# Performance work log

Hardware: AMD Instinct MI355X
Metric: run time of the kernel (lower is better)

## Reference

```python
import jax, jax.numpy as jnp
import numpy as np

B, T, E, D = 64, 512, 1024, 1024  # batch, enc timesteps, enc hidden, dec hidden


def setup_inputs() -> dict:
    key = jax.random.key(0)
    ks = jax.random.split(key, 9)
    s = lambda fan_in: 1.0 / np.sqrt(fan_in)
    return {
        "hidden": jax.random.normal(ks[0], (B, D), jnp.float32),
        "decoder_out": jax.random.normal(ks[1], (B, D), jnp.float32),
        "encoder_states": jax.random.normal(ks[2], (T, B, E), jnp.float32),
        # attn: Linear(D+E -> 2E)
        "Wa": jax.random.uniform(ks[3], (2 * E, D + E), jnp.float32, -s(D + E), s(D + E)),
        "ba": jax.random.uniform(ks[4], (2 * E,), jnp.float32, -s(D + E), s(D + E)),
        # attn2: Linear(2E -> 1)
        "w2": jax.random.uniform(ks[5], (1, 2 * E), jnp.float32, -s(2 * E), s(2 * E)),
        "b2": jax.random.uniform(ks[6], (1,), jnp.float32, -s(2 * E), s(2 * E)),
        # attn_combine: Linear(D+E -> D)
        "Wc": jax.random.uniform(ks[7], (D, D + E), jnp.float32, -s(D + E), s(D + E)),
        "bc": jax.random.uniform(ks[8], (D,), jnp.float32, -s(D + E), s(D + E)),
    }


def reference(hidden, decoder_out, encoder_states, Wa, ba, w2, b2, Wc, bc):
    d = hidden.shape[1]
    # attn(cat(hidden, enc_t)) = hidden @ Wa[:, :D].T + enc_t @ Wa[:, D:].T + ba
    h_proj = hidden @ Wa[:, :d].T + ba                      # [B, 2E]
    e_proj = jnp.einsum('tbe,fe->tbf', encoder_states, Wa[:, d:])  # [T, B, 2E]
    act = jnp.tanh(h_proj[None, :, :] + e_proj)             # [T, B, 2E]
    scores = jnp.einsum('tbf,f->bt', act, w2[0]) + b2[0]    # [B, T]
    weights = jax.nn.softmax(scores, axis=-1)               # softmax over timesteps
    # weighted sum of encoder states: [B, E]
    applied = jnp.einsum('bt,tbe->be', weights, encoder_states)
    combined = jnp.concatenate([decoder_out, applied], axis=1)  # [B, D+E]
    out = jnp.tanh(combined @ Wc.T + bc)                    # [B, D]
    return out, applied
```

## Files before the change

### kernel.cpp

```cpp
#include <hip/hip_runtime.h>
#include <hip/hip_bf16.h>

#define BB 64
#define TT 512
#define EE 1024
#define DD 1024

typedef __attribute__((ext_vector_type(8))) short s16x8;
typedef __attribute__((ext_vector_type(4))) float f32x4;

#define AS1 __attribute__((address_space(1)))
#define AS3 __attribute__((address_space(3)))

__device__ __forceinline__ unsigned short f2bf(float f) {
    unsigned int u = __builtin_bit_cast(unsigned int, f);
    u += 0x7FFF + ((u >> 16) & 1);
    return (unsigned short)(u >> 16);
}
__device__ __forceinline__ float tanh_fast(float x) {
    x = fminf(fmaxf(x, -15.f), 15.f);
    float e = __expf(2.f * x);
    return (e - 1.f) / (e + 1.f);
}

__device__ __forceinline__ int tile_slot(int row, int g) {
    return (row >> 4) * 128 + (g >> 2) * 64 + (g & 3) * 16 + (row & 15);
}

__global__ __launch_bounds__(256) void conv_encS_kernel(
    const float* __restrict__ enc, unsigned short* __restrict__ encS)
{
    __shared__ short tileL[1024 * 8];
    const int tm  = blockIdx.x;
    const int tk  = blockIdx.y;
    const int tid = threadIdx.x;

#pragma unroll
    for (int it = 0; it < 4; ++it) {
        int cidx = it * 256 + tid;
        int row  = cidx >> 3;
        int g    = cidx & 7;
        const float* src = enc + (size_t)(tm * 128 + row) * 1024 + tk * 64 + g * 8;
        float4 v0 = ((const float4*)src)[0];
        float4 v1 = ((const float4*)src)[1];
        short c[8];
        c[0] = (short)f2bf(v0.x); c[1] = (short)f2bf(v0.y);
        c[2] = (short)f2bf(v0.z); c[3] = (short)f2bf(v0.w);
        c[4] = (short)f2bf(v1.x); c[5] = (short)f2bf(v1.y);
        c[6] = (short)f2bf(v1.z); c[7] = (short)f2bf(v1.w);
        *(s16x8*)&tileL[tile_slot(row, g) * 8] = *(s16x8*)c;
    }
    __syncthreads();
    unsigned short* dst = encS + ((size_t)tm * 16 + tk) * 8192;
#pragma unroll
    for (int it = 0; it < 4; ++it) {
        int s = it * 256 + tid;
        *(s16x8*)&dst[s * 8] = *(const s16x8*)&tileL[s * 8];
    }
}

__global__ __launch_bounds__(256) void prep_kernel(
    const float* __restrict__ Wa,
    const float* __restrict__ hidden,
    const float* __restrict__ ba,
    unsigned short* __restrict__ WaS,
    float* __restrict__ hp)
{
    __shared__ float smem[8 * 1024];
    const int bid = blockIdx.x;
    const int tid = threadIdx.x;

    if (bid < 256) {
        short* tileL = (short*)smem;
        const int tn = bid & 15;
        const int tk = bid >> 4;
#pragma unroll
        for (int it = 0; it < 4; ++it) {
            int cidx = it * 256 + tid;
            int row  = cidx >> 3;
            int g    = cidx & 7;
            const float* src = Wa + (size_t)(tn * 128 + row) * 2048 + 1024 + tk * 64 + g * 8;
            float4 v0 = ((const float4*)src)[0];
            float4 v1 = ((const float4*)src)[1];
            short c[8];
            c[0] = (short)f2bf(v0.x); c[1] = (short)f2bf(v0.y);
            c[2] = (short)f2bf(v0.z); c[3] = (short)f2bf(v0.w);
            c[4] = (short)f2bf(v1.x); c[5] = (short)f2bf(v1.y);
            c[6] = (short)f2bf(v1.z); c[7] = (short)f2bf(v1.w);
            *(s16x8*)&tileL[tile_slot(row, g) * 8] = *(s16x8*)c;
        }
        __syncthreads();
        unsigned short* dst = WaS + ((size_t)tn * 16 + tk) * 8192;
#pragma unroll
        for (int it = 0; it < 4; ++it) {
            int s = it * 256 + tid;
            *(s16x8*)&dst[s * 8] = *(const s16x8*)&tileL[s * 8];
        }
    } else {
        const int lane = tid & 63;
        const int wave = tid >> 6;
        const int f0   = (bid - 256) * 8;
#pragma unroll
        for (int i = 0; i < 8; ++i) {
            int idx = i * 256 + tid;
            int fi  = idx >> 8;
            int c4  = idx & 255;
            ((float4*)smem)[idx] = *(const float4*)(Wa + (size_t)(f0 + fi) * 2048 + c4 * 4);
        }
        __syncthreads();
        for (int bi = 0; bi < 16; ++bi) {
            int b = wave * 16 + bi;
            float h[16];
#pragma unroll
            for (int j = 0; j < 16; ++j) h[j] = hidden[b * 1024 + lane + 64 * j];
#pragma unroll
            for (int fi = 0; fi < 8; ++fi) {
                float s = 0.f;
#pragma unroll
                for (int j = 0; j < 16; ++j) s += h[j] * smem[fi * 1024 + lane + 64 * j];
#pragma unroll
                for (int m = 32; m; m >>= 1) s += __shfl_xor(s, m);
                if (lane == 0) hp[(f0 + fi) * 64 + b] = s + ba[f0 + fi];
            }
        }
    }
}

__global__ __launch_bounds__(1024) void gemm_scores(
    const unsigned short* __restrict__ encS,
    const unsigned short* __restrict__ WaS,
    const float* __restrict__ hp,
    const float* __restrict__ w2,
    float* __restrict__ scoresP)
{
    __shared__ short sA[2][2][8192];
    __shared__ short sB[2][2][8192];
    __shared__ float rowAcc[256];

    const int tid  = threadIdx.x;
    const int bid  = blockIdx.x;
    const int w    = (bid & 7) * 128 + (bid >> 3);
    const int bm   = w >> 3;
    const int bn   = w & 7;
    const int lane = tid & 63;
    const int wave = tid >> 6;
    const int wm   = wave >> 2;
    const int wn   = wave & 3;
    const int c    = lane & 15;
    const int quad = lane >> 4;
    const int mt   = wm >> 1;
    const int mrow0 = (wm & 1) * 4;
    const int nt   = wn >> 1;
    const int nrow0 = (wn & 1) * 4;

    f32x4 acc[4][4];
#pragma unroll
    for (int m = 0; m < 4; ++m)
#pragma unroll
        for (int n = 0; n < 4; ++n)
#pragma unroll
            for (int r = 0; r < 4; ++r) acc[m][n][r] = 0.f;

    const unsigned short* aT = encS + ((size_t)(bm * 2) * 16) * 8192;
    const unsigned short* bT = WaS  + ((size_t)(bn * 2) * 16) * 8192;

    auto STAGE_ALL = [&](int kt, int nb) {
#pragma unroll
        for (int t = 0; t < 2; ++t) {
            const unsigned short* sa = aT + ((size_t)(t * 16 + kt)) * 8192;
            __builtin_amdgcn_global_load_lds(
                (const AS1 void*)(sa + tid * 8),
                (AS3 void*)&sA[nb][t][tid * 8], 16, 0, 0);
            const unsigned short* sb = bT + ((size_t)(t * 16 + kt)) * 8192;
            __builtin_amdgcn_global_load_lds(
                (const AS1 void*)(sb + tid * 8),
                (AS3 void*)&sB[nb][t][tid * 8], 16, 0, 0);
        }
    };

    STAGE_ALL(0, 0);

    for (int kt = 0; kt < 16; ++kt) {
        const int cur = kt & 1;
        asm volatile("s_waitcnt vmcnt(0)" ::: "memory");
        __builtin_amdgcn_s_barrier();
        __builtin_amdgcn_sched_barrier(0);
        if (kt < 15) STAGE_ALL(kt + 1, cur ^ 1);

#pragma unroll
        for (int kk = 0; kk < 2; ++kk) {
            s16x8 aF[4], bF[4];
#pragma unroll
            for (int m = 0; m < 4; ++m)
                aF[m] = *(const s16x8*)
                    &sA[cur][mt][((mrow0 + m) * 128 + kk * 64 + lane) * 8];
#pragma unroll
            for (int n = 0; n < 4; ++n)
                bF[n] = *(const s16x8*)
                    &sB[cur][nt][((nrow0 + n) * 128 + kk * 64 + lane) * 8];

            __builtin_amdgcn_s_setprio(1);
#pragma unroll
            for (int m = 0; m < 4; ++m)
#pragma unroll
                for (int n = 0; n < 4; ++n)
                    acc[m][n] = __builtin_amdgcn_mfma_f32_16x16x32_bf16(
                        aF[m], bF[n], acc[m][n], 0, 0, 0);
            __builtin_amdgcn_s_setprio(0);
        }
        __builtin_amdgcn_sched_barrier(0);
        __builtin_amdgcn_s_barrier();
    }

    if (tid < 256) rowAcc[tid] = 0.f;
    __syncthreads();

    float w2v[4];
#pragma unroll
    for (int n = 0; n < 4; ++n) w2v[n] = w2[bn * 256 + wn * 64 + n * 16 + c];

#pragma unroll
    for (int m = 0; m < 4; ++m) {
        int lrow0 = wm * 64 + m * 16 + quad * 4;
        int b0    = lrow0 & 63;
        f32x4 hp4[4];
#pragma unroll
        for (int n = 0; n < 4; ++n)
            hp4[n] = *(const f32x4*)&hp[(bn * 256 + wn * 64 + n * 16 + c) * 64 + b0];
#pragma unroll
        for (int r = 0; r < 4; ++r) {
            float s = 0.f;
#pragma unroll
            for (int n = 0; n < 4; ++n)
                s += tanh_fast(acc[m][n][r] + hp4[n][r]) * w2v[n];
            s += __shfl_xor(s, 1);
            s += __shfl_xor(s, 2);
            s += __shfl_xor(s, 4);
            s += __shfl_xor(s, 8);
            if (c == 0) atomicAdd(&rowAcc[lrow0 + r], s);
        }
    }
    __syncthreads();
    if (tid < 256) {
        int b = tid & 63;
        int t = bm * 4 + (tid >> 6);
        scoresP[((size_t)bn * 64 + b) * 512 + t] = rowAcc[tid];
    }
}

__global__ __launch_bounds__(256) void applied_part_kernel(
    const float* __restrict__ enc,
    const float* __restrict__ scoresP,
    float* __restrict__ part)
{
    __shared__ float red[128 * 8];
    __shared__ float sw[512];
    __shared__ float red4[4];
    const int tc  = blockIdx.x;
    const int b   = blockIdx.y;
    const int tid = threadIdx.x;
    const int eo  = tid & 127;
    const int th  = tid >> 7;
    const int e0  = eo * 8;

    {
        const int t0 = tid * 2;
        float s0 = 0.f, s1 = 0.f;
#pragma unroll
        for (int bn = 0; bn < 8; ++bn) {
            const float* sp = scoresP + ((size_t)bn * 64 + b) * 512;
            s0 += sp[t0]; s1 += sp[t0 + 1];
        }
        float m = fmaxf(s0, s1);
#pragma unroll
        for (int o = 32; o; o >>= 1) m = fmaxf(m, __shfl_xor(m, o));
        if ((tid & 63) == 0) red4[tid >> 6] = m;
        __syncthreads();
        m = fmaxf(fmaxf(red4[0], red4[1]), fmaxf(red4[2], red4[3]));
        __syncthreads();
        float e0v = __expf(s0 - m), e1v = __expf(s1 - m);
        float ss = e0v + e1v;
#pragma unroll
        for (int o = 32; o; o >>= 1) ss += __shfl_xor(ss, o);
        if ((tid & 63) == 0) red4[tid >> 6] = ss;
        __syncthreads();
        float inv = 1.f / (red4[0] + red4[1] + red4[2] + red4[3]);
        sw[t0]     = e0v * inv;
        sw[t0 + 1] = e1v * inv;
        __syncthreads();
    }

    float a[8];
#pragma unroll
    for (int j = 0; j < 8; ++j) a[j] = 0.f;

    for (int it = 0; it < 16; ++it) {
        int t = tc * 32 + th * 16 + it;
        float wt = sw[t];
        const float* src = enc + ((size_t)(t * BB + b)) * EE + e0;
        float4 v0 = ((const float4*)src)[0];
        float4 v1 = ((const float4*)src)[1];
        a[0] += wt * v0.x; a[1] += wt * v0.y; a[2] += wt * v0.z; a[3] += wt * v0.w;
        a[4] += wt * v1.x; a[5] += wt * v1.y; a[6] += wt * v1.z; a[7] += wt * v1.w;
    }
    if (th == 1) {
#pragma unroll
        for (int j = 0; j < 8; ++j) red[eo * 8 + j] = a[j];
    }
    __syncthreads();
    if (th == 0) {
        float* dst = part + ((size_t)tc * 64 + b) * 1024 + e0;
#pragma unroll
        for (int j = 0; j < 8; ++j) dst[j] = a[j] + red[eo * 8 + j];
    }
}

__global__ __launch_bounds__(256) void applied_reduce_kernel(
    const float* __restrict__ part, float* __restrict__ out_applied)
{
    int idx = blockIdx.x * 256 + threadIdx.x;
    float s = 0.f;
#pragma unroll
    for (int tc = 0; tc < 16; ++tc) s += part[tc * 65536 + idx];
    out_applied[idx] = s;
}

__global__ __launch_bounds__(256) void combine_kernel(
    const float* __restrict__ dec,
    const float* applied,
    const float* __restrict__ Wc,
    const float* __restrict__ bc,
    float* out0)
{
    const int gw   = blockIdx.x * 4 + (threadIdx.x >> 6);
    const int lane = threadIdx.x & 63;
    const int d0   = (gw >> 3) * 8;
    const int b0   = (gw & 7) * 8;

    float acc[8][8];
#pragma unroll
    for (int dd = 0; dd < 8; ++dd)
#pragma unroll
        for (int bb = 0; bb < 8; ++bb) acc[dd][bb] = 0.f;

#pragma unroll
    for (int j = 0; j < 8; ++j) {
        float4 wv[8];
#pragma unroll
        for (int dd = 0; dd < 8; ++dd)
            wv[dd] = ((const float4*)(Wc + (size_t)(d0 + dd) * 2048))[j * 64 + lane];
        float4 cv[8];
        if (j < 4) {
#pragma unroll
            for (int bb = 0; bb < 8; ++bb)
                cv[bb] = ((const float4*)(dec + (size_t)(b0 + bb) * 1024))[j * 64 + lane];
        } else {
#pragma unroll
            for (int bb = 0; bb < 8; ++bb)
                cv[bb] = ((const float4*)(applied + (size_t)(b0 + bb) * 1024))[(j - 4) * 64 + lane];
        }
#pragma unroll
        for (int dd = 0; dd < 8; ++dd)
#pragma unroll
            for (int bb = 0; bb < 8; ++bb)
                acc[dd][bb] += wv[dd].x * cv[bb].x + wv[dd].y * cv[bb].y
                             + wv[dd].z * cv[bb].z + wv[dd].w * cv[bb].w;
    }

#pragma unroll
    for (int dd = 0; dd < 8; ++dd) {
#pragma unroll
        for (int bb = 0; bb < 8; ++bb) {
            float s = acc[dd][bb];
#pragma unroll
            for (int m = 32; m; m >>= 1) s += __shfl_xor(s, m);
            if (lane == 0)
                out0[(size_t)(b0 + bb) * DD + d0 + dd] = tanh_fast(s + bc[d0 + dd]);
        }
    }
}

extern "C" void kernel_launch(void* const* d_in, const int* in_sizes, int n_in,
                              void* d_out, int out_size, void* d_ws, size_t ws_size,
                              hipStream_t stream) {
    const float* hidden = (const float*)d_in[0];
    const float* dec    = (const float*)d_in[1];
    const float* enc    = (const float*)d_in[2];
    const float* Wa     = (const float*)d_in[3];
    const float* ba     = (const float*)d_in[4];
    const float* w2     = (const float*)d_in[5];
    const float* Wc     = (const float*)d_in[7];
    const float* bc     = (const float*)d_in[8];
    float* out = (float*)d_out;

    unsigned short* encS = (unsigned short*)d_ws;
    unsigned short* WaS  = encS + (size_t)33554432;
    float* hp      = (float*)(WaS + (size_t)2097152);
    float* scoresP = hp + 131072;
    float* part    = scoresP + 262144;

    dim3 gc(256, 16);
    conv_encS_kernel<<<gc, 256, 0, stream>>>(enc, encS);
    prep_kernel<<<512, 256, 0, stream>>>(Wa, hidden, ba, WaS, hp);
    gemm_scores<<<1024, 1024, 0, stream>>>(encS, WaS, hp, w2, scoresP);
    dim3 g3(16, 64);
    applied_part_kernel<<<g3, 256, 0, stream>>>(enc, scoresP, part);
    applied_reduce_kernel<<<256, 256, 0, stream>>>(part, out + BB * DD);
    combine_kernel<<<256, 256, 0, stream>>>(dec, out + BB * DD, Wc, bc, out);
}
```

Before: 515.2 us.

## Fuse encoder fp32-to-bf16 conversion into GEMM A-tile staging

Removes the separate conversion kernel that wrote a bf16 swizzled copy of encoder_states to workspace. The GEMM now loads fp32 encoder rows into registers, converts them to bf16 and writes them into LDS in the swizzled tile layout, pipelined one k-step ahead. B tiles still use direct global-to-LDS loads. This avoids a full extra write and read pass over the 128 MB encoder tensor, in exchange for doubled A global traffic per GEMM block (fp32, and each A tile is reread by the 8 N-blocks), extra register pressure and conversion ALU work inside the main loop.

```diff
diff --git a/kernel.cpp b/kernel.cpp
--- a/kernel.cpp
+++ b/kernel.cpp
@@ -25,38 +25,6 @@
 
 __device__ __forceinline__ int tile_slot(int row, int g) {
     return (row >> 4) * 128 + (g >> 2) * 64 + (g & 3) * 16 + (row & 15);
-}
-
-__global__ __launch_bounds__(256) void conv_encS_kernel(
-    const float* __restrict__ enc, unsigned short* __restrict__ encS)
-{
-    __shared__ short tileL[1024 * 8];
-    const int tm  = blockIdx.x;
-    const int tk  = blockIdx.y;
-    const int tid = threadIdx.x;
-
-#pragma unroll
-    for (int it = 0; it < 4; ++it) {
-        int cidx = it * 256 + tid;
-        int row  = cidx >> 3;
-        int g    = cidx & 7;
-        const float* src = enc + (size_t)(tm * 128 + row) * 1024 + tk * 64 + g * 8;
-        float4 v0 = ((const float4*)src)[0];
-        float4 v1 = ((const float4*)src)[1];
-        short c[8];
-        c[0] = (short)f2bf(v0.x); c[1] = (short)f2bf(v0.y);
-        c[2] = (short)f2bf(v0.z); c[3] = (short)f2bf(v0.w);
-        c[4] = (short)f2bf(v1.x); c[5] = (short)f2bf(v1.y);
-        c[6] = (short)f2bf(v1.z); c[7] = (short)f2bf(v1.w);
-        *(s16x8*)&tileL[tile_slot(row, g) * 8] = *(s16x8*)c;
-    }
-    __syncthreads();
-    unsigned short* dst = encS + ((size_t)tm * 16 + tk) * 8192;
-#pragma unroll
-    for (int it = 0; it < 4; ++it) {
-        int s = it * 256 + tid;
-        *(s16x8*)&dst[s * 8] = *(const s16x8*)&tileL[s * 8];
-    }
 }
 
 __global__ __launch_bounds__(256) void prep_kernel(
@@ -127,7 +95,7 @@
 }
 
 __global__ __launch_bounds__(1024) void gemm_scores(
-    const unsigned short* __restrict__ encS,
+    const float* __restrict__ enc,
     const unsigned short* __restrict__ WaS,
     const float* __restrict__ hp,
     const float* __restrict__ w2,
@@ -153,6 +121,11 @@
     const int nt   = wn >> 1;
     const int nrow0 = (wn & 1) * 4;
 
+    const int arow  = tid >> 3;
+    const int ag    = tid & 7;
+    const int aslot = tile_slot(arow, ag) * 8;
+    const float* aBase = enc + ((size_t)(bm * 256) + arow) * 1024 + ag * 8;
+
     f32x4 acc[4][4];
 #pragma unroll
     for (int m = 0; m < 4; ++m)
@@ -161,16 +134,32 @@
 #pragma unroll
             for (int r = 0; r < 4; ++r) acc[m][n][r] = 0.f;
 
-    const unsigned short* aT = encS + ((size_t)(bm * 2) * 16) * 8192;
-    const unsigned short* bT = WaS  + ((size_t)(bn * 2) * 16) * 8192;
-
-    auto STAGE_ALL = [&](int kt, int nb) {
+    const unsigned short* bT = WaS + ((size_t)(bn * 2) * 16) * 8192;
+
+    float4 pa[2][2];
+
+    auto A_LOAD = [&](int kt) {
 #pragma unroll
         for (int t = 0; t < 2; ++t) {
-            const unsigned short* sa = aT + ((size_t)(t * 16 + kt)) * 8192;
-            __builtin_amdgcn_global_load_lds(
-                (const AS1 void*)(sa + tid * 8),
-                (AS3 void*)&sA[nb][t][tid * 8], 16, 0, 0);
+            const float* s = aBase + (size_t)t * 131072 + kt * 64;
+            pa[t][0] = ((const float4*)s)[0];
+            pa[t][1] = ((const float4*)s)[1];
+        }
+    };
+    auto A_WRITE = [&](int nb) {
+#pragma unroll
+        for (int t = 0; t < 2; ++t) {
+            short cv[8];
+            cv[0] = (short)f2bf(pa[t][0].x); cv[1] = (short)f2bf(pa[t][0].y);
+            cv[2] = (short)f2bf(pa[t][0].z); cv[3] = (short)f2bf(pa[t][0].w);
+            cv[4] = (short)f2bf(pa[t][1].x); cv[5] = (short)f2bf(pa[t][1].y);
+            cv[6] = (short)f2bf(pa[t][1].z); cv[7] = (short)f2bf(pa[t][1].w);
+            *(s16x8*)&sA[nb][t][aslot] = *(s16x8*)cv;
+        }
+    };
+    auto B_STAGE = [&](int kt, int nb) {
+#pragma unroll
+        for (int t = 0; t < 2; ++t) {
             const unsigned short* sb = bT + ((size_t)(t * 16 + kt)) * 8192;
             __builtin_amdgcn_global_load_lds(
                 (const AS1 void*)(sb + tid * 8),
@@ -178,14 +167,21 @@
         }
     };
 
-    STAGE_ALL(0, 0);
+    A_LOAD(0);
+    B_STAGE(0, 0);
+    A_WRITE(0);
 
     for (int kt = 0; kt < 16; ++kt) {
         const int cur = kt & 1;
         asm volatile("s_waitcnt vmcnt(0)" ::: "memory");
+        asm volatile("s_waitcnt lgkmcnt(0)" ::: "memory");
         __builtin_amdgcn_s_barrier();
         __builtin_amdgcn_sched_barrier(0);
-        if (kt < 15) STAGE_ALL(kt + 1, cur ^ 1);
+
+        if (kt < 15) {
+            A_LOAD(kt + 1);
+            B_STAGE(kt + 1, cur ^ 1);
+        }
 
 #pragma unroll
         for (int kk = 0; kk < 2; ++kk) {
@@ -208,10 +204,15 @@
                         aF[m], bF[n], acc[m][n], 0, 0, 0);
             __builtin_amdgcn_s_setprio(0);
         }
-        __builtin_amdgcn_sched_barrier(0);
-        __builtin_amdgcn_s_barrier();
-    }
-
+
+        if (kt < 15) {
+            asm volatile("s_waitcnt vmcnt(2)" ::: "memory");
+            __builtin_amdgcn_sched_barrier(0);
+            A_WRITE(cur ^ 1);
+        }
+    }
+
+    __syncthreads();
     if (tid < 256) rowAcc[tid] = 0.f;
     __syncthreads();
 
@@ -393,16 +394,13 @@
     const float* bc     = (const float*)d_in[8];
     float* out = (float*)d_out;
 
-    unsigned short* encS = (unsigned short*)d_ws;
-    unsigned short* WaS  = encS + (size_t)33554432;
+    unsigned short* WaS = (unsigned short*)d_ws;
     float* hp      = (float*)(WaS + (size_t)2097152);
     float* scoresP = hp + 131072;
     float* part    = scoresP + 262144;
 
-    dim3 gc(256, 16);
-    conv_encS_kernel<<<gc, 256, 0, stream>>>(enc, encS);
     prep_kernel<<<512, 256, 0, stream>>>(Wa, hidden, ba, WaS, hp);
-    gemm_scores<<<1024, 1024, 0, stream>>>(encS, WaS, hp, w2, scoresP);
+    gemm_scores<<<1024, 1024, 0, stream>>>(enc, WaS, hp, w2, scoresP);
     dim3 g3(16, 64);
     applied_part_kernel<<<g3, 256, 0, stream>>>(enc, scoresP, part);
     applied_reduce_kernel<<<256, 256, 0, stream>>>(part, out + BB * DD);
```

Result: no change. 507.0 us (-1.6%).
